# Performance work log

Measured on AMD Instinct MI355X. Metric: run time of the kernel, lower is better.

## Reference

```python
import jax, jax.numpy as jnp
import numpy as np

B, H, W, C = 2, 128, 128, 128
K = 3            # window_size
NB = K * K       # neighbor_count = 9
RP = 8           # relative_position_dim
HID = 128        # edge hidden = max(256//2, 128)
EIN = 3 * C + RP # edge_input_dim = 392
CLIP = 3.0
GEPS = 1e-06     # gate_eps
LNE = 1e-05      # LayerNorm eps


def _ln(x, g, b):
    m = x.mean(-1, keepdims=True)
    v = ((x - m) ** 2).mean(-1, keepdims=True)
    return (x - m) * jax.lax.rsqrt(v + LNE) * g + b


def setup_inputs() -> dict:
    key = jax.random.key(0)
    ks = jax.random.split(key, 12)
    f32 = jnp.float32
    inp = {
        'tokens': jax.random.normal(ks[0], (B, H, W, C), dtype=f32),
        'ln1_g': jnp.ones((C,), f32), 'ln1_b': jnp.zeros((C,), f32),
        'ln2_g': jnp.ones((C,), f32), 'ln2_b': jnp.zeros((C,), f32),
        'rel_pos': 0.02 * jax.random.normal(ks[1], (NB, RP), dtype=f32),
        'dW1': 0.01 * jax.random.normal(ks[2], (EIN, HID), dtype=f32),
        'db1': jnp.zeros((HID,), f32),
        'dW2': 0.01 * jax.random.normal(ks[3], (HID, 1), dtype=f32),
        'db2': jnp.zeros((1,), f32),
        'rW1': 0.01 * jax.random.normal(ks[4], (EIN, HID), dtype=f32),
        'rb1': jnp.zeros((HID,), f32),
        'rW2': 0.01 * jax.random.normal(ks[5], (HID, 1), dtype=f32),
        'rb2': jnp.zeros((1,), f32),
        'vW': 0.01 * jax.random.normal(ks[6], (C, C), dtype=f32),
        'vb': jnp.zeros((C,), f32),
        'oW': 0.01 * jax.random.normal(ks[7], (C, C), dtype=f32),
        'ob': jnp.zeros((C,), f32),
        'eml_gamma': jnp.asarray(0.1, f32),
        'eml_lam': jnp.asarray(1.0, f32),
        'eml_bias': jnp.asarray(-0.3, f32),
    }
    return inp


def _edge_mlp(x, W1, b1, W2, b2):
    h = jax.nn.gelu(jnp.einsum('blnd,dh->blnh', x, W1) + b1, approximate=False)
    return jnp.einsum('blnh,ho->blno', h, W2) + b2


def _forward(tokens, ln1_g, ln1_b, ln2_g, ln2_b, rel_pos, dW1, db1, dW2, db2,
             rW1, rb1, rW2, rb2, vW, vb, oW, ob, eml_gamma, eml_lam, eml_bias,
             warmup_eta=1.0):
    Bh, Hh, Wh, Ch = tokens.shape
    L = Hh * Wh
    normalized = _ln(tokens, ln1_g, ln1_b)
    flat = normalized.reshape(Bh, L, Ch)
    # Unfold(kernel=3, padding=1): gather 9 shifted views, then replicate torch's
    # reshape of the (C, 9)-ordered channel axis into (9, C).
    pad = jnp.pad(normalized, ((0, 0), (1, 1), (1, 1), (0, 0)))
    shifts = [pad[:, i:i + Hh, j:j + Wh, :] for i in range(K) for j in range(K)]
    nbhd = jnp.stack(shifts, axis=-1)                       # [B,H,W,C,9]
    nbhd = nbhd.reshape(Bh, L, Ch * NB).reshape(Bh, L, NB, Ch)  # torch reshape semantics
    center = jnp.broadcast_to(flat[:, :, None, :], nbhd.shape)
    rel = jnp.broadcast_to(rel_pos[None, None], (Bh, L, NB, rel_pos.shape[-1]))
    edge_features = jnp.concatenate([center, nbhd, center - nbhd, rel], axis=-1)
    drive = _edge_mlp(edge_features, dW1, db1, dW2, db2)[..., 0]        # [B,L,9]
    resistance = _edge_mlp(edge_features, rW1, rb1, rW2, rb2)[..., 0]   # [B,L,9]
    # EML unit (Ohm's-law style gate): clamp(eta*gamma*drive/(lambda*softplus(R)+eps)+bias)
    energy = jnp.clip(
        warmup_eta * (eml_gamma * drive) / (eml_lam * jax.nn.softplus(resistance) + GEPS)
        + eml_bias, -CLIP, CLIP)
    gate = jax.nn.sigmoid(energy)                                        # [B,L,9]
    values = jnp.einsum('blnc,cd->blnd', nbhd, vW) + vb                  # [B,L,9,C]
    gate_mass = jnp.maximum(gate.sum(axis=2), GEPS)                      # [B,L]
    message = jnp.einsum('bln,blnc->blc', gate, values) / gate_mass[..., None]
    update = (jnp.einsum('blc,cd->bld', message, oW) + ob).reshape(Bh, Hh, Wh, Ch)
    output = _ln(tokens + update, ln2_g, ln2_b)  # dropout is identity at eval
    return output


def reference(tokens, ln1_g, ln1_b, ln2_g, ln2_b, rel_pos, dW1, db1, dW2, db2,
              rW1, rb1, rW2, rb2, vW, vb, oW, ob, eml_gamma, eml_lam, eml_bias):
    return _forward(tokens, ln1_g, ln1_b, ln2_g, ln2_b, rel_pos, dW1, db1, dW2, db2,
                    rW1, rb1, rW2, rb2, vW, vb, oW, ob, eml_gamma, eml_lam, eml_bias)
```

## Files before the change

kernel.cpp:

```cpp
#include <hip/hip_runtime.h>


#define USHORT unsigned short
#define AS_W 168
#define W_W  160

typedef __attribute__((ext_vector_type(8)))  __bf16 v8bf;
typedef __attribute__((ext_vector_type(8)))  USHORT v8u;
typedef __attribute__((ext_vector_type(16))) float  v16f;

__device__ __forceinline__ float bflo(unsigned u) {
    unsigned v = u << 16; float f; __builtin_memcpy(&f, &v, 4); return f;
}
__device__ __forceinline__ float bfhi(unsigned u) {
    unsigned v = u & 0xffff0000u; float f; __builtin_memcpy(&f, &v, 4); return f;
}
__device__ __forceinline__ USHORT f2bf(float f) {
    unsigned v; __builtin_memcpy(&v, &f, 4);
    v += 0x7FFFu + ((v >> 16) & 1u);
    return (USHORT)(v >> 16);
}

__global__ __launch_bounds__(256) void k_prep(
    const float* __restrict__ dW1, const float* __restrict__ db1,
    const float* __restrict__ rW1, const float* __restrict__ rb1,
    const float* __restrict__ rel, const float* __restrict__ dW2,
    const float* __restrict__ rW2, const float* __restrict__ vW,
    const float* __restrict__ vb,  const float* __restrict__ oW,
    USHORT* __restrict__ WnTg, USHORT* __restrict__ WcTg, USHORT* __restrict__ VTg,
    float* __restrict__ preg, float* __restrict__ vboWg, float* __restrict__ w2g)
{
    const int blk = blockIdx.x, t = threadIdx.x;
    if (blk < 72) {
        int idx = blk * 256 + t;
        int n = ((idx >> 4) * 7282) >> 16;
        int k = idx - n * 144;
        int r = k >> 4, tt = k & 15, c2 = r + 9 * tt;
        float acc = 0.f;
        if (c2 < 128)
            for (int j = 0; j < 128; ++j) acc += vW[c2 * 128 + j] * oW[j * 128 + n];
        VTg[idx] = f2bf(acc);
    } else if (blk < 216) {
        int idx = (blk - 72) * 256 + t;
        int n = ((idx >> 4) * 7282) >> 16;
        int k = idx - n * 144;
        int r = k >> 4, tt = k & 15, c2 = r + 9 * tt;
        int col = n & 127;
        const float* W = (n < 128) ? dW1 : rW1;
        float val = 0.f;
        if (c2 < 128) val = W[(128 + c2) * 128 + col] - W[(256 + c2) * 128 + col];
        WnTg[idx] = f2bf(val);
    } else if (blk < 344) {
        int idx = (blk - 216) * 256 + t;
        int n = idx >> 7, c = idx & 127, col = n & 127;
        const float* W = (n < 128) ? dW1 : rW1;
        WcTg[idx] = f2bf(W[c * 128 + col] + W[(256 + c) * 128 + col]);
    } else if (blk < 353) {
        int n2 = blk - 344; int h = t;
        float acc;
        if (h < 128) {
            acc = db1[h];
            for (int r = 0; r < 8; ++r) acc += rel[n2 * 8 + r] * dW1[(384 + r) * 128 + h];
        } else {
            int hh = h - 128;
            acc = rb1[hh];
            for (int r = 0; r < 8; ++r) acc += rel[n2 * 8 + r] * rW1[(384 + r) * 128 + hh];
        }
        preg[n2 * 256 + h] = acc;
    } else {
        if (t < 128) {
            float acc = 0.f;
            for (int j = 0; j < 128; ++j) acc += vb[j] * oW[j * 128 + t];
            vboWg[t] = acc;
            w2g[t] = dW2[t];
            w2g[128 + t] = rW2[t];
        }
    }
}

__global__ __launch_bounds__(256) void k_ln1(
    const float* __restrict__ tok, const float* __restrict__ g,
    const float* __restrict__ b, USHORT* __restrict__ nb)
{
    const int p = blockIdx.x * 4 + (threadIdx.x >> 6);
    const int lane = threadIdx.x & 63;
    const float2 x = ((const float2*)(tok + (size_t)p * 128))[lane];
    float s = x.x + x.y;
    for (int m = 1; m < 64; m <<= 1) s += __shfl_xor(s, m);
    const float mean = s * (1.f / 128.f);
    const float d0 = x.x - mean, d1 = x.y - mean;
    float q = d0 * d0 + d1 * d1;
    for (int m = 1; m < 64; m <<= 1) q += __shfl_xor(q, m);
    const float rstd = rsqrtf(q * (1.f / 128.f) + 1e-5f);
    const float2 gg = ((const float2*)g)[lane], bb = ((const float2*)b)[lane];
    const float o0 = d0 * rstd * gg.x + bb.x;
    const float o1 = d1 * rstd * gg.y + bb.y;
    ((unsigned*)nb)[(size_t)p * 64 + lane] =
        (unsigned)f2bf(o0) | ((unsigned)f2bf(o1) << 16);
}

__device__ __forceinline__ void gather_tile(
    USHORT* __restrict__ Ash, const USHORT* __restrict__ nb,
    int n2, int y, int bI, int tid)
{
    const int x = tid >> 2, q = tid & 3;
    #pragma unroll
    for (int r = 0; r < 9; ++r) {
        int u = 2 * n2 + r;
        int n = (u >= 18) ? (u - 18) : ((u >= 9) ? (u - 9) : u);
        int v = n2 * 128 + r;
        int c0 = (v * 7282) >> 16;
        int dyq = (n * 22) >> 6;
        int dx = n - 3 * dyq - 1;
        int dy = dyq - 1;
        int sy = y + dy, sx = x + dx;
        bool ok = ((unsigned)sy < 128u) && ((unsigned)sx < 128u);
        int e0 = (c0 & ~1) + 4 * q;
        size_t gidx = ((size_t)((bI * 128 + (ok ? sy : 0)) * 128 + (ok ? sx : 0))) * 128 + e0;
        const unsigned* gp = (const unsigned*)nb + (gidx >> 1);
        unsigned dw0 = gp[0], dw1 = gp[1];
        unsigned nxt = (unsigned)__shfl_down((int)dw0, 1);
        unsigned o0, o1;
        if (c0 & 1) { o0 = (dw0 >> 16) | (dw1 << 16); o1 = (dw1 >> 16) | (nxt << 16); }
        else        { o0 = dw0;                       o1 = dw1; }
        if (!ok) { o0 = 0u; o1 = 0u; }
        *(uint2*)(Ash + x * AS_W + 16 * r + 4 * q) = make_uint2(o0, o1);
    }
}

__global__ __launch_bounds__(512, 2) void k_edge(
    const float* __restrict__ tok, const float* __restrict__ ln2g,
    const float* __restrict__ ln2b, const USHORT* __restrict__ nb,
    const USHORT* __restrict__ WnTg, const USHORT* __restrict__ WcTg,
    const USHORT* __restrict__ VTg, const float* __restrict__ preg,
    const float* __restrict__ vboWg, const float* __restrict__ w2g,
    const float* __restrict__ db2p, const float* __restrict__ rb2p,
    const float* __restrict__ gmp, const float* __restrict__ lmp,
    const float* __restrict__ bip, const float* __restrict__ obp,
    float* __restrict__ out)
{
    extern __shared__ char smem[];
    USHORT* Wsh  = (USHORT*)smem;
    USHORT* Ash  = (USHORT*)(smem + 81920);
    float*  preL = (float*)(smem + 124928);
    float*  w2L  = (float*)(smem + 134144);
    float*  dsum = (float*)(smem + 135168);
    float*  rsum = (float*)(smem + 135680);
    float*  gateL= (float*)(smem + 136192);
    float*  sgL  = (float*)(smem + 136704);

    const int tid = threadIdx.x;
    const int lane = tid & 63, wave = tid >> 6, hi = lane >> 5, l31 = lane & 31;
    const int mw = wave & 1, nw = wave >> 1;
    const int blk = blockIdx.x;
    const int bI = blk >> 7;
    const int y = ((blk & 7) << 4) | ((blk >> 3) & 15);
    const int p0 = (bI * 128 + y) * 128;

    for (int i = tid; i < 4096; i += 512) {
        int n = i >> 4, kv = i & 15;
        *(v8u*)(Wsh + n * W_W + kv * 8) = *(const v8u*)(WcTg + n * 128 + kv * 8);
    }
    for (int i = tid; i < 2048; i += 512) {
        int x = i >> 4, kv = i & 15;
        *(v8u*)(Ash + x * AS_W + kv * 8) = *(const v8u*)(nb + (size_t)(p0 + x) * 128 + kv * 8);
    }
    for (int i = tid; i < 2304; i += 512) preL[i] = preg[i];
    if (tid < 256) w2L[tid] = w2g[tid];
    if (tid < 128) { dsum[tid] = 0.f; rsum[tid] = 0.f; sgL[tid] = 0.f; }
    __syncthreads();

    v16f cp[2][2];
    #pragma unroll
    for (int a = 0; a < 2; ++a)
        for (int b = 0; b < 2; ++b)
            for (int e = 0; e < 16; ++e) cp[a][b][e] = 0.f;
    #pragma unroll
    for (int ks = 0; ks < 8; ++ks) {
        v8bf af0 = *(const v8bf*)(Ash + (mw * 64 + l31) * AS_W + ks * 16 + hi * 8);
        v8bf af1 = *(const v8bf*)(Ash + (mw * 64 + 32 + l31) * AS_W + ks * 16 + hi * 8);
        v8bf bf0 = *(const v8bf*)(Wsh + (nw * 64 + l31) * W_W + ks * 16 + hi * 8);
        v8bf bf1 = *(const v8bf*)(Wsh + (nw * 64 + 32 + l31) * W_W + ks * 16 + hi * 8);
        cp[0][0] = __builtin_amdgcn_mfma_f32_32x32x16_bf16(af0, bf0, cp[0][0], 0, 0, 0);
        cp[0][1] = __builtin_amdgcn_mfma_f32_32x32x16_bf16(af0, bf1, cp[0][1], 0, 0, 0);
        cp[1][0] = __builtin_amdgcn_mfma_f32_32x32x16_bf16(af1, bf0, cp[1][0], 0, 0, 0);
        cp[1][1] = __builtin_amdgcn_mfma_f32_32x32x16_bf16(af1, bf1, cp[1][1], 0, 0, 0);
    }
    __syncthreads();

    for (int i = tid; i < 4608; i += 512) {
        int n = (i * 3641) >> 16;
        int kv = i - n * 18;
        *(v8u*)(Wsh + n * W_W + kv * 8) = *(const v8u*)(WnTg + n * 144 + kv * 8);
    }
    gather_tile(Ash, nb, 0, y, bI, tid);

    const float gmv = gmp[0], lmv = lmp[0], biv = bip[0];
    const float db2v = db2p[0], rb2v = rb2p[0];

    float wn[36];
    #pragma unroll
    for (int i = 0; i < 36; ++i) wn[i] = 0.f;

    for (int n2 = 0; n2 < 9; ++n2) {
        __syncthreads();
        v16f acc[2][2];
        #pragma unroll
        for (int a = 0; a < 2; ++a)
            for (int b = 0; b < 2; ++b) acc[a][b] = cp[a][b];
        #pragma unroll
        for (int ks = 0; ks < 9; ++ks) {
            v8bf af0 = *(const v8bf*)(Ash + (mw * 64 + l31) * AS_W + ks * 16 + hi * 8);
            v8bf af1 = *(const v8bf*)(Ash + (mw * 64 + 32 + l31) * AS_W + ks * 16 + hi * 8);
            v8bf bf0 = *(const v8bf*)(Wsh + (nw * 64 + l31) * W_W + ks * 16 + hi * 8);
            v8bf bf1 = *(const v8bf*)(Wsh + (nw * 64 + 32 + l31) * W_W + ks * 16 + hi * 8);
            acc[0][0] = __builtin_amdgcn_mfma_f32_32x32x16_bf16(af0, bf0, acc[0][0], 0, 0, 0);
            acc[0][1] = __builtin_amdgcn_mfma_f32_32x32x16_bf16(af0, bf1, acc[0][1], 0, 0, 0);
            acc[1][0] = __builtin_amdgcn_mfma_f32_32x32x16_bf16(af1, bf0, acc[1][0], 0, 0, 0);
            acc[1][1] = __builtin_amdgcn_mfma_f32_32x32x16_bf16(af1, bf1, acc[1][1], 0, 0, 0);
        }
        #pragma unroll
        for (int mt = 0; mt < 2; ++mt) {
            float part[16];
            #pragma unroll
            for (int rr = 0; rr < 16; ++rr) part[rr] = 0.f;
            #pragma unroll
            for (int nt = 0; nt < 2; ++nt) {
                int col = nw * 64 + nt * 32 + l31;
                float pv = preL[n2 * 256 + col];
                float wv = w2L[col];
                #pragma unroll
                for (int rr = 0; rr < 16; ++rr) {
                    float h = acc[mt][nt][rr] + pv;
                    float sg = __builtin_amdgcn_rcpf(1.f + __expf(-1.702f * h));
                    part[rr] += h * sg * wv;
                }
            }
            #pragma unroll
            for (int m = 1; m < 32; m <<= 1) {
                #pragma unroll
                for (int rr = 0; rr < 16; ++rr) part[rr] += __shfl_xor(part[rr], m);
            }
            if (l31 == 0) {
                float* tgt = (nw < 2) ? dsum : rsum;
                #pragma unroll
                for (int rr = 0; rr < 16; ++rr) {
                    int row = mw * 64 + mt * 32 + (rr & 3) + 8 * (rr >> 2) + 4 * hi;
                    atomicAdd(&tgt[row], part[rr]);
                }
            }
        }
        __syncthreads();
        if (tid < 128) {
            float d = dsum[tid] + db2v, rr = rsum[tid] + rb2v;
            float sp = fmaxf(rr, 0.f) + log1pf(__expf(-fabsf(rr)));
            float e = gmv * d / (lmv * sp + 1e-6f) + biv;
            e = fminf(fmaxf(e, -3.f), 3.f);
            float gt = 1.f / (1.f + __expf(-e));
            gateL[tid] = gt; sgL[tid] += gt;
            dsum[tid] = 0.f; rsum[tid] = 0.f;
        }
        __syncthreads();
        {
            int x = tid >> 2, q = tid & 3;
            float gt = gateL[x];
            const USHORT* rp = Ash + x * AS_W + q * 36;
            #pragma unroll
            for (int j = 0; j < 9; ++j) {
                uint2 pk = *(const uint2*)(rp + 4 * j);
                wn[4 * j + 0] += gt * bflo(pk.x);
                wn[4 * j + 1] += gt * bfhi(pk.x);
                wn[4 * j + 2] += gt * bflo(pk.y);
                wn[4 * j + 3] += gt * bfhi(pk.y);
            }
        }
        __syncthreads();
        if (n2 < 8) gather_tile(Ash, nb, n2 + 1, y, bI, tid);
    }

    {
        int x = tid >> 2, q = tid & 3;
        USHORT* wp = Ash + x * AS_W + q * 36;
        #pragma unroll
        for (int j = 0; j < 9; ++j) {
            unsigned lo = (unsigned)f2bf(wn[4 * j + 0]) | ((unsigned)f2bf(wn[4 * j + 1]) << 16);
            unsigned h2 = (unsigned)f2bf(wn[4 * j + 2]) | ((unsigned)f2bf(wn[4 * j + 3]) << 16);
            *(uint2*)(wp + 4 * j) = make_uint2(lo, h2);
        }
    }
    for (int i = tid; i < 2304; i += 512) {
        int n = (i * 3641) >> 16;
        int kv = i - n * 18;
        *(v8u*)(Wsh + n * W_W + kv * 8) = *(const v8u*)(VTg + n * 144 + kv * 8);
    }
    if (tid < 128) {
        float s = sgL[tid];
        float m = fmaxf(s, 1e-6f);
        dsum[tid] = 1.f / m;
        rsum[tid] = s / m;
    }
    __syncthreads();

    v16f a3[2];
    #pragma unroll
    for (int a = 0; a < 2; ++a)
        for (int e = 0; e < 16; ++e) a3[a][e] = 0.f;
    #pragma unroll
    for (int ks = 0; ks < 9; ++ks) {
        v8bf bf0 = *(const v8bf*)(Wsh + (nw * 32 + l31) * W_W + ks * 16 + hi * 8);
        v8bf af0 = *(const v8bf*)(Ash + (mw * 64 + l31) * AS_W + ks * 16 + hi * 8);
        v8bf af1 = *(const v8bf*)(Ash + (mw * 64 + 32 + l31) * AS_W + ks * 16 + hi * 8);
        a3[0] = __builtin_amdgcn_mfma_f32_32x32x16_bf16(af0, bf0, a3[0], 0, 0, 0);
        a3[1] = __builtin_amdgcn_mfma_f32_32x32x16_bf16(af1, bf0, a3[1], 0, 0, 0);
    }
    __syncthreads();

    float* updF = (float*)smem;
    {
        int colc = nw * 32 + l31;
        float vbw = vboWg[colc], obv = obp[colc];
        #pragma unroll
        for (int mt = 0; mt < 2; ++mt) {
            #pragma unroll
            for (int rr = 0; rr < 16; ++rr) {
                int row = mw * 64 + mt * 32 + (rr & 3) + 8 * (rr >> 2) + 4 * hi;
                updF[row * 128 + colc] = a3[mt][rr] * dsum[row] + vbw * rsum[row] + obv;
            }
        }
    }
    __syncthreads();

    const float g20 = ln2g[lane], g21 = ln2g[lane + 64];
    const float b20 = ln2b[lane], b21 = ln2b[lane + 64];
    for (int q2 = 0; q2 < 16; ++q2) {
        int p = wave * 16 + q2;
        size_t gp = (size_t)(p0 + p) * 128;
        float x0 = tok[gp + lane]      + updF[p * 128 + lane];
        float x1 = tok[gp + lane + 64] + updF[p * 128 + lane + 64];
        float s = x0 + x1;
        for (int m = 1; m < 64; m <<= 1) s += __shfl_xor(s, m);
        float mean = s * (1.f / 128.f);
        float d0 = x0 - mean, d1 = x1 - mean;
        float qq = d0 * d0 + d1 * d1;
        for (int m = 1; m < 64; m <<= 1) qq += __shfl_xor(qq, m);
        float rstd = rsqrtf(qq * (1.f / 128.f) + 1e-5f);
        out[gp + lane]      = d0 * rstd * g20 + b20;
        out[gp + lane + 64] = d1 * rstd * g21 + b21;
    }
}

extern "C" void kernel_launch(void* const* d_in, const int* in_sizes, int n_in,
                              void* d_out, int out_size, void* d_ws, size_t ws_size,
                              hipStream_t stream) {
    const float* tok  = (const float*)d_in[0];
    const float* ln1g = (const float*)d_in[1];
    const float* ln1b = (const float*)d_in[2];
    const float* ln2g = (const float*)d_in[3];
    const float* ln2b = (const float*)d_in[4];
    const float* rel  = (const float*)d_in[5];
    const float* dW1  = (const float*)d_in[6];
    const float* db1  = (const float*)d_in[7];
    const float* dW2  = (const float*)d_in[8];
    const float* db2  = (const float*)d_in[9];
    const float* rW1  = (const float*)d_in[10];
    const float* rb1  = (const float*)d_in[11];
    const float* rW2  = (const float*)d_in[12];
    const float* rb2  = (const float*)d_in[13];
    const float* vW   = (const float*)d_in[14];
    const float* vb   = (const float*)d_in[15];
    const float* oW   = (const float*)d_in[16];
    const float* ob   = (const float*)d_in[17];
    const float* gm   = (const float*)d_in[18];
    const float* lm   = (const float*)d_in[19];
    const float* bi   = (const float*)d_in[20];
    float* out = (float*)d_out;

    char* w = (char*)d_ws;
    USHORT* norm = (USHORT*)w; w += 8388608;
    USHORT* WnTg = (USHORT*)w; w += 73728;
    USHORT* WcTg = (USHORT*)w; w += 65536;
    USHORT* VTg  = (USHORT*)w; w += 36864;
    float*  preg = (float*)w;  w += 9216;
    float*  vboWg= (float*)w;  w += 512;
    float*  w2g  = (float*)w;  w += 1024;

    hipFuncSetAttribute((const void*)k_edge,
                        hipFuncAttributeMaxDynamicSharedMemorySize, 137216);

    hipLaunchKernelGGL(k_prep, dim3(354), dim3(256), 0, stream,
                       dW1, db1, rW1, rb1, rel, dW2, rW2, vW, vb, oW,
                       WnTg, WcTg, VTg, preg, vboWg, w2g);
    hipLaunchKernelGGL(k_ln1, dim3(8192), dim3(256), 0, stream,
                       tok, ln1g, ln1b, norm);
    hipLaunchKernelGGL(k_edge, dim3(256), dim3(512), 137216, stream,
                       tok, ln2g, ln2b, norm, WnTg, WcTg, VTg, preg, vboWg, w2g,
                       db2, rb2, gm, lm, bi, ob, out);
}
```

Measured before the change: 223.3 us.

## Fold gated value projection into per-neighbor MFMA and merge prep with LN1

Instead of building a gate-weighted neighbor sum in registers (36 floats per thread) and running a final value/output MFMA on it, each neighbor iteration now multiplies the gathered tile by the fused V·O weight with MFMA and accumulates gate-scaled results into accumulators. The V weight stays resident in a new LDS region, preg is read from global instead of LDS, and the gather for the next neighbor is issued right after the MFMAs. The LN1 kernel is merged into the weight-prep kernel to save a launch. This adds 9x extra MFMA work and raises LDS use to about 155KB. That still fits 1 block/CU, but the launch bound of 2 blocks is impossible at this size.

```diff
diff --git a/kernel.cpp b/kernel.cpp
--- a/kernel.cpp
+++ b/kernel.cpp
@@ -2,35 +2,48 @@
 
 
 #define USHORT unsigned short
-#define AS_W 168
-#define W_W  160
+#define AW 152
 
 typedef __attribute__((ext_vector_type(8)))  __bf16 v8bf;
 typedef __attribute__((ext_vector_type(8)))  USHORT v8u;
 typedef __attribute__((ext_vector_type(16))) float  v16f;
 
-__device__ __forceinline__ float bflo(unsigned u) {
-    unsigned v = u << 16; float f; __builtin_memcpy(&f, &v, 4); return f;
-}
-__device__ __forceinline__ float bfhi(unsigned u) {
-    unsigned v = u & 0xffff0000u; float f; __builtin_memcpy(&f, &v, 4); return f;
-}
 __device__ __forceinline__ USHORT f2bf(float f) {
     unsigned v; __builtin_memcpy(&v, &f, 4);
     v += 0x7FFFu + ((v >> 16) & 1u);
     return (USHORT)(v >> 16);
 }
 
-__global__ __launch_bounds__(256) void k_prep(
+__global__ __launch_bounds__(256) void k_setup(
+    const float* __restrict__ tok, const float* __restrict__ ln1g,
+    const float* __restrict__ ln1b,
     const float* __restrict__ dW1, const float* __restrict__ db1,
     const float* __restrict__ rW1, const float* __restrict__ rb1,
     const float* __restrict__ rel, const float* __restrict__ dW2,
     const float* __restrict__ rW2, const float* __restrict__ vW,
     const float* __restrict__ vb,  const float* __restrict__ oW,
+    USHORT* __restrict__ norm,
     USHORT* __restrict__ WnTg, USHORT* __restrict__ WcTg, USHORT* __restrict__ VTg,
     float* __restrict__ preg, float* __restrict__ vboWg, float* __restrict__ w2g)
 {
     const int blk = blockIdx.x, t = threadIdx.x;
+    if (blk >= 354) {
+        const int p = (blk - 354) * 4 + (t >> 6);
+        const int lane = t & 63;
+        const float2 x = ((const float2*)(tok + (size_t)p * 128))[lane];
+        float s = x.x + x.y;
+        for (int m = 1; m < 64; m <<= 1) s += __shfl_xor(s, m);
+        const float mean = s * (1.f / 128.f);
+        const float d0 = x.x - mean, d1 = x.y - mean;
+        float q = d0 * d0 + d1 * d1;
+        for (int m = 1; m < 64; m <<= 1) q += __shfl_xor(q, m);
+        const float rstd = rsqrtf(q * (1.f / 128.f) + 1e-5f);
+        const float2 gg = ((const float2*)ln1g)[lane], bb = ((const float2*)ln1b)[lane];
+        ((unsigned*)norm)[(size_t)p * 64 + lane] =
+            (unsigned)f2bf(d0 * rstd * gg.x + bb.x) |
+            ((unsigned)f2bf(d1 * rstd * gg.y + bb.y) << 16);
+        return;
+    }
     if (blk < 72) {
         int idx = blk * 256 + t;
         int n = ((idx >> 4) * 7282) >> 16;
@@ -78,27 +91,6 @@
     }
 }
 
-__global__ __launch_bounds__(256) void k_ln1(
-    const float* __restrict__ tok, const float* __restrict__ g,
-    const float* __restrict__ b, USHORT* __restrict__ nb)
-{
-    const int p = blockIdx.x * 4 + (threadIdx.x >> 6);
-    const int lane = threadIdx.x & 63;
-    const float2 x = ((const float2*)(tok + (size_t)p * 128))[lane];
-    float s = x.x + x.y;
-    for (int m = 1; m < 64; m <<= 1) s += __shfl_xor(s, m);
-    const float mean = s * (1.f / 128.f);
-    const float d0 = x.x - mean, d1 = x.y - mean;
-    float q = d0 * d0 + d1 * d1;
-    for (int m = 1; m < 64; m <<= 1) q += __shfl_xor(q, m);
-    const float rstd = rsqrtf(q * (1.f / 128.f) + 1e-5f);
-    const float2 gg = ((const float2*)g)[lane], bb = ((const float2*)b)[lane];
-    const float o0 = d0 * rstd * gg.x + bb.x;
-    const float o1 = d1 * rstd * gg.y + bb.y;
-    ((unsigned*)nb)[(size_t)p * 64 + lane] =
-        (unsigned)f2bf(o0) | ((unsigned)f2bf(o1) << 16);
-}
-
 __device__ __forceinline__ void gather_tile(
     USHORT* __restrict__ Ash, const USHORT* __restrict__ nb,
     int n2, int y, int bI, int tid)
@@ -124,7 +116,7 @@
         if (c0 & 1) { o0 = (dw0 >> 16) | (dw1 << 16); o1 = (dw1 >> 16) | (nxt << 16); }
         else        { o0 = dw0;                       o1 = dw1; }
         if (!ok) { o0 = 0u; o1 = 0u; }
-        *(uint2*)(Ash + x * AS_W + 16 * r + 4 * q) = make_uint2(o0, o1);
+        *(uint2*)(Ash + x * AW + 16 * r + 4 * q) = make_uint2(o0, o1);
     }
 }
 
@@ -141,13 +133,14 @@
 {
     extern __shared__ char smem[];
     USHORT* Wsh  = (USHORT*)smem;
-    USHORT* Ash  = (USHORT*)(smem + 81920);
-    float*  preL = (float*)(smem + 124928);
-    float*  w2L  = (float*)(smem + 134144);
-    float*  dsum = (float*)(smem + 135168);
-    float*  rsum = (float*)(smem + 135680);
-    float*  gateL= (float*)(smem + 136192);
-    float*  sgL  = (float*)(smem + 136704);
+    USHORT* Ash  = (USHORT*)(smem + 77824);
+    USHORT* VTl  = (USHORT*)(smem + 116736);
+    float*  w2L  = (float*)(smem + 155648);
+    float*  dsum = (float*)(smem + 156672);
+    float*  rsum = (float*)(smem + 157184);
+    float*  gateL= (float*)(smem + 157696);
+    float*  sgL  = (float*)(smem + 158208);
+    float*  updF = (float*)smem;
 
     const int tid = threadIdx.x;
     const int lane = tid & 63, wave = tid >> 6, hi = lane >> 5, l31 = lane & 31;
@@ -159,13 +152,17 @@
 
     for (int i = tid; i < 4096; i += 512) {
         int n = i >> 4, kv = i & 15;
-        *(v8u*)(Wsh + n * W_W + kv * 8) = *(const v8u*)(WcTg + n * 128 + kv * 8);
+        *(v8u*)(Wsh + n * AW + kv * 8) = *(const v8u*)(WcTg + n * 128 + kv * 8);
     }
     for (int i = tid; i < 2048; i += 512) {
         int x = i >> 4, kv = i & 15;
-        *(v8u*)(Ash + x * AS_W + kv * 8) = *(const v8u*)(nb + (size_t)(p0 + x) * 128 + kv * 8);
-    }
-    for (int i = tid; i < 2304; i += 512) preL[i] = preg[i];
+        *(v8u*)(Ash + x * AW + kv * 8) = *(const v8u*)(nb + (size_t)(p0 + x) * 128 + kv * 8);
+    }
+    for (int i = tid; i < 2304; i += 512) {
+        int n = (i * 3641) >> 16;
+        int kv = i - n * 18;
+        *(v8u*)(VTl + n * AW + kv * 8) = *(const v8u*)(VTg + n * 144 + kv * 8);
+    }
     if (tid < 256) w2L[tid] = w2g[tid];
     if (tid < 128) { dsum[tid] = 0.f; rsum[tid] = 0.f; sgL[tid] = 0.f; }
     __syncthreads();
@@ -177,10 +174,10 @@
             for (int e = 0; e < 16; ++e) cp[a][b][e] = 0.f;
     #pragma unroll
     for (int ks = 0; ks < 8; ++ks) {
-        v8bf af0 = *(const v8bf*)(Ash + (mw * 64 + l31) * AS_W + ks * 16 + hi * 8);
-        v8bf af1 = *(const v8bf*)(Ash + (mw * 64 + 32 + l31) * AS_W + ks * 16 + hi * 8);
-        v8bf bf0 = *(const v8bf*)(Wsh + (nw * 64 + l31) * W_W + ks * 16 + hi * 8);
-        v8bf bf1 = *(const v8bf*)(Wsh + (nw * 64 + 32 + l31) * W_W + ks * 16 + hi * 8);
+        v8bf af0 = *(const v8bf*)(Ash + (mw * 64 + l31) * AW + ks * 16 + hi * 8);
+        v8bf af1 = *(const v8bf*)(Ash + (mw * 64 + 32 + l31) * AW + ks * 16 + hi * 8);
+        v8bf bf0 = *(const v8bf*)(Wsh + (nw * 64 + l31) * AW + ks * 16 + hi * 8);
+        v8bf bf1 = *(const v8bf*)(Wsh + (nw * 64 + 32 + l31) * AW + ks * 16 + hi * 8);
         cp[0][0] = __builtin_amdgcn_mfma_f32_32x32x16_bf16(af0, bf0, cp[0][0], 0, 0, 0);
         cp[0][1] = __builtin_amdgcn_mfma_f32_32x32x16_bf16(af0, bf1, cp[0][1], 0, 0, 0);
         cp[1][0] = __builtin_amdgcn_mfma_f32_32x32x16_bf16(af1, bf0, cp[1][0], 0, 0, 0);
@@ -191,18 +188,23 @@
     for (int i = tid; i < 4608; i += 512) {
         int n = (i * 3641) >> 16;
         int kv = i - n * 18;
-        *(v8u*)(Wsh + n * W_W + kv * 8) = *(const v8u*)(WnTg + n * 144 + kv * 8);
+        *(v8u*)(Wsh + n * AW + kv * 8) = *(const v8u*)(WnTg + n * 144 + kv * 8);
     }
     gather_tile(Ash, nb, 0, y, bI, tid);
 
     const float gmv = gmp[0], lmv = lmp[0], biv = bip[0];
     const float db2v = db2p[0], rb2v = rb2p[0];
-
-    float wn[36];
+    const float wv0 = w2L[nw * 64 + l31];
+    const float wv1 = w2L[nw * 64 + 32 + l31];
+
+    v16f acc3[2];
     #pragma unroll
-    for (int i = 0; i < 36; ++i) wn[i] = 0.f;
+    for (int a = 0; a < 2; ++a)
+        for (int e = 0; e < 16; ++e) acc3[a][e] = 0.f;
 
     for (int n2 = 0; n2 < 9; ++n2) {
+        const float pv0 = preg[n2 * 256 + nw * 64 + l31];
+        const float pv1 = preg[n2 * 256 + nw * 64 + 32 + l31];
         __syncthreads();
         v16f acc[2][2];
         #pragma unroll
@@ -210,10 +212,10 @@
             for (int b = 0; b < 2; ++b) acc[a][b] = cp[a][b];
         #pragma unroll
         for (int ks = 0; ks < 9; ++ks) {
-            v8bf af0 = *(const v8bf*)(Ash + (mw * 64 + l31) * AS_W + ks * 16 + hi * 8);
-            v8bf af1 = *(const v8bf*)(Ash + (mw * 64 + 32 + l31) * AS_W + ks * 16 + hi * 8);
-            v8bf bf0 = *(const v8bf*)(Wsh + (nw * 64 + l31) * W_W + ks * 16 + hi * 8);
-            v8bf bf1 = *(const v8bf*)(Wsh + (nw * 64 + 32 + l31) * W_W + ks * 16 + hi * 8);
+            v8bf af0 = *(const v8bf*)(Ash + (mw * 64 + l31) * AW + ks * 16 + hi * 8);
+            v8bf af1 = *(const v8bf*)(Ash + (mw * 64 + 32 + l31) * AW + ks * 16 + hi * 8);
+            v8bf bf0 = *(const v8bf*)(Wsh + (nw * 64 + l31) * AW + ks * 16 + hi * 8);
+            v8bf bf1 = *(const v8bf*)(Wsh + (nw * 64 + 32 + l31) * AW + ks * 16 + hi * 8);
             acc[0][0] = __builtin_amdgcn_mfma_f32_32x32x16_bf16(af0, bf0, acc[0][0], 0, 0, 0);
             acc[0][1] = __builtin_amdgcn_mfma_f32_32x32x16_bf16(af0, bf1, acc[0][1], 0, 0, 0);
             acc[1][0] = __builtin_amdgcn_mfma_f32_32x32x16_bf16(af1, bf0, acc[1][0], 0, 0, 0);
@@ -223,18 +225,12 @@
         for (int mt = 0; mt < 2; ++mt) {
             float part[16];
             #pragma unroll
-            for (int rr = 0; rr < 16; ++rr) part[rr] = 0.f;
-            #pragma unroll
-            for (int nt = 0; nt < 2; ++nt) {
-                int col = nw * 64 + nt * 32 + l31;
-                float pv = preL[n2 * 256 + col];
-                float wv = w2L[col];
-                #pragma unroll
-                for (int rr = 0; rr < 16; ++rr) {
-                    float h = acc[mt][nt][rr] + pv;
-                    float sg = __builtin_amdgcn_rcpf(1.f + __expf(-1.702f * h));
-                    part[rr] += h * sg * wv;
-                }
+            for (int rr = 0; rr < 16; ++rr) {
+                float h0 = acc[mt][0][rr] + pv0;
+                float h1 = acc[mt][1][rr] + pv1;
+                float s0 = __builtin_amdgcn_rcpf(1.f + __expf(-1.702f * h0));
+                float s1 = __builtin_amdgcn_rcpf(1.f + __expf(-1.702f * h1));
+                part[rr] = h0 * s0 * wv0 + h1 * s1 * wv1;
             }
             #pragma unroll
             for (int m = 1; m < 32; m <<= 1) {
@@ -250,7 +246,20 @@
                 }
             }
         }
+        v16f P[2];
+        #pragma unroll
+        for (int a = 0; a < 2; ++a)
+            for (int e = 0; e < 16; ++e) P[a][e] = 0.f;
+        #pragma unroll
+        for (int ks = 0; ks < 9; ++ks) {
+            v8bf af0 = *(const v8bf*)(Ash + (mw * 64 + l31) * AW + ks * 16 + hi * 8);
+            v8bf af1 = *(const v8bf*)(Ash + (mw * 64 + 32 + l31) * AW + ks * 16 + hi * 8);
+            v8bf vf  = *(const v8bf*)(VTl + (nw * 32 + l31) * AW + ks * 16 + hi * 8);
+            P[0] = __builtin_amdgcn_mfma_f32_32x32x16_bf16(af0, vf, P[0], 0, 0, 0);
+            P[1] = __builtin_amdgcn_mfma_f32_32x32x16_bf16(af1, vf, P[1], 0, 0, 0);
+        }
         __syncthreads();
+        if (n2 < 8) gather_tile(Ash, nb, n2 + 1, y, bI, tid);
         if (tid < 128) {
             float d = dsum[tid] + db2v, rr = rsum[tid] + rb2v;
             float sp = fmaxf(rr, 0.f) + log1pf(__expf(-fabsf(rr)));
@@ -261,38 +270,17 @@
             dsum[tid] = 0.f; rsum[tid] = 0.f;
         }
         __syncthreads();
-        {
-            int x = tid >> 2, q = tid & 3;
-            float gt = gateL[x];
-            const USHORT* rp = Ash + x * AS_W + q * 36;
+        #pragma unroll
+        for (int mt = 0; mt < 2; ++mt) {
+            const float4* gq = (const float4*)&gateL[mw * 64 + mt * 32 + 4 * hi];
+            float4 ga = gq[0], gb = gq[2], gc = gq[4], gd = gq[6];
+            float gs[16] = {ga.x, ga.y, ga.z, ga.w, gb.x, gb.y, gb.z, gb.w,
+                            gc.x, gc.y, gc.z, gc.w, gd.x, gd.y, gd.z, gd.w};
             #pragma unroll
-            for (int j = 0; j < 9; ++j) {
-                uint2 pk = *(const uint2*)(rp + 4 * j);
-                wn[4 * j + 0] += gt * bflo(pk.x);
-                wn[4 * j + 1] += gt * bfhi(pk.x);
-                wn[4 * j + 2] += gt * bflo(pk.y);
-                wn[4 * j + 3] += gt * bfhi(pk.y);
-            }
-        }
-        __syncthreads();
-        if (n2 < 8) gather_tile(Ash, nb, n2 + 1, y, bI, tid);
-    }
-
-    {
-        int x = tid >> 2, q = tid & 3;
-        USHORT* wp = Ash + x * AS_W + q * 36;
-        #pragma unroll
-        for (int j = 0; j < 9; ++j) {
-            unsigned lo = (unsigned)f2bf(wn[4 * j + 0]) | ((unsigned)f2bf(wn[4 * j + 1]) << 16);
-            unsigned h2 = (unsigned)f2bf(wn[4 * j + 2]) | ((unsigned)f2bf(wn[4 * j + 3]) << 16);
-            *(uint2*)(wp + 4 * j) = make_uint2(lo, h2);
-        }
-    }
-    for (int i = tid; i < 2304; i += 512) {
-        int n = (i * 3641) >> 16;
-        int kv = i - n * 18;
-        *(v8u*)(Wsh + n * W_W + kv * 8) = *(const v8u*)(VTg + n * 144 + kv * 8);
-    }
+            for (int rr = 0; rr < 16; ++rr) acc3[mt][rr] += gs[rr] * P[mt][rr];
+        }
+    }
+
     if (tid < 128) {
         float s = sgL[tid];
         float m = fmaxf(s, 1e-6f);
@@ -301,30 +289,24 @@
     }
     __syncthreads();
 
-    v16f a3[2];
-    #pragma unroll
-    for (int a = 0; a < 2; ++a)
-        for (int e = 0; e < 16; ++e) a3[a][e] = 0.f;
-    #pragma unroll
-    for (int ks = 0; ks < 9; ++ks) {
-        v8bf bf0 = *(const v8bf*)(Wsh + (nw * 32 + l31) * W_W + ks * 16 + hi * 8);
-        v8bf af0 = *(const v8bf*)(Ash + (mw * 64 + l31) * AS_W + ks * 16 + hi * 8);
-        v8bf af1 = *(const v8bf*)(Ash + (mw * 64 + 32 + l31) * AS_W + ks * 16 + hi * 8);
-        a3[0] = __builtin_amdgcn_mfma_f32_32x32x16_bf16(af0, bf0, a3[0], 0, 0, 0);
-        a3[1] = __builtin_amdgcn_mfma_f32_32x32x16_bf16(af1, bf0, a3[1], 0, 0, 0);
-    }
-    __syncthreads();
-
-    float* updF = (float*)smem;
     {
-        int colc = nw * 32 + l31;
-        float vbw = vboWg[colc], obv = obp[colc];
+        const int colc = nw * 32 + l31;
+        const float vbw = vboWg[colc], obv = obp[colc];
         #pragma unroll
         for (int mt = 0; mt < 2; ++mt) {
+            const int base = mw * 64 + mt * 32 + 4 * hi;
+            const float4* iq = (const float4*)&dsum[base];
+            const float4* sq = (const float4*)&rsum[base];
+            float4 ia = iq[0], ib = iq[2], ic = iq[4], id = iq[6];
+            float4 sa = sq[0], sb = sq[2], sc = sq[4], sd = sq[6];
+            float iv[16] = {ia.x, ia.y, ia.z, ia.w, ib.x, ib.y, ib.z, ib.w,
+                            ic.x, ic.y, ic.z, ic.w, id.x, id.y, id.z, id.w};
+            float sv[16] = {sa.x, sa.y, sa.z, sa.w, sb.x, sb.y, sb.z, sb.w,
+                            sc.x, sc.y, sc.z, sc.w, sd.x, sd.y, sd.z, sd.w};
             #pragma unroll
             for (int rr = 0; rr < 16; ++rr) {
-                int row = mw * 64 + mt * 32 + (rr & 3) + 8 * (rr >> 2) + 4 * hi;
-                updF[row * 128 + colc] = a3[mt][rr] * dsum[row] + vbw * rsum[row] + obv;
+                int row = base + (rr & 3) + 8 * (rr >> 2);
+                updF[row * 128 + colc] = acc3[mt][rr] * iv[rr] + vbw * sv[rr] + obv;
             }
         }
     }
@@ -385,14 +367,12 @@
     float*  w2g  = (float*)w;  w += 1024;
 
     hipFuncSetAttribute((const void*)k_edge,
-                        hipFuncAttributeMaxDynamicSharedMemorySize, 137216);
-
-    hipLaunchKernelGGL(k_prep, dim3(354), dim3(256), 0, stream,
-                       dW1, db1, rW1, rb1, rel, dW2, rW2, vW, vb, oW,
-                       WnTg, WcTg, VTg, preg, vboWg, w2g);
-    hipLaunchKernelGGL(k_ln1, dim3(8192), dim3(256), 0, stream,
-                       tok, ln1g, ln1b, norm);
-    hipLaunchKernelGGL(k_edge, dim3(256), dim3(512), 137216, stream,
+                        hipFuncAttributeMaxDynamicSharedMemorySize, 158720);
+
+    hipLaunchKernelGGL(k_setup, dim3(8546), dim3(256), 0, stream,
+                       tok, ln1g, ln1b, dW1, db1, rW1, rb1, rel, dW2, rW2,
+                       vW, vb, oW, norm, WnTg, WcTg, VTg, preg, vboWg, w2g);
+    hipLaunchKernelGGL(k_edge, dim3(256), dim3(512), 158720, stream,
                        tok, ln2g, ln2b, norm, WnTg, WcTg, VTg, preg, vboWg, w2g,
                        db2, rb2, gm, lm, bi, ob, out);
 }
```

Measured after the change: 209.8 us. -6.1%, faster.
